# Optimization experiments

Measured on AMD Instinct MI355X. Metric: run time of the kernel, lower is better.

Reference implementation:

```python
import jax, jax.numpy as jnp
import numpy as np

N = 100000      # nodes
E = 1600000     # edges (before self-loops)
IN = 128        # in_channels
HID = 64        # hidden_channels (= out_channels)
HEADS = 8
CH = HID // HEADS  # per-head channels in GAT (concat=True)


def setup_inputs() -> dict:
    key = jax.random.key(0)
    ks = jax.random.split(key, 12)
    s = 0.1  # param init scale
    return {
        "x": jax.random.normal(ks[0], (N, IN), jnp.float32),
        "edge_index": jax.random.randint(ks[1], (2, E), 0, N, dtype=jnp.int32),
        # GCNConv 0: in -> hid
        "W0": s * jax.random.normal(ks[2], (IN, HID), jnp.float32),
        "b0": jnp.zeros((HID,), jnp.float32),
        # GATConv: hid -> heads x ch (concat)
        "Wg": s * jax.random.normal(ks[3], (HID, HEADS * CH), jnp.float32),
        "att_src": s * jax.random.normal(ks[4], (HEADS, CH), jnp.float32),
        "att_dst": s * jax.random.normal(ks[5], (HEADS, CH), jnp.float32),
        "bg": jnp.zeros((HEADS * CH,), jnp.float32),
        # GCNConv 2: hid -> hid
        "W2": s * jax.random.normal(ks[6], (HID, HID), jnp.float32),
        "b2": jnp.zeros((HID,), jnp.float32),
        # GCNConv 3 (final): hid -> out
        "W3": s * jax.random.normal(ks[7], (HID, HID), jnp.float32),
        "b3": jnp.zeros((HID,), jnp.float32),
    }


def _gcn_conv(x, src, dst, W, b, n):
    deg = jax.ops.segment_sum(jnp.ones(src.shape[0], x.dtype), dst, num_segments=n)
    dinv = jnp.where(deg > 0, jax.lax.rsqrt(deg), 0.0)
    h = x @ W                                  # [n, out]
    norm = dinv[src] * dinv[dst]               # [e]
    msg = h[src] * norm[:, None]               # gather + scale
    return jax.ops.segment_sum(msg, dst, num_segments=n) + b


def _gat_conv(x, src, dst, W, a_src, a_dst, b, n):
    # PyG GATConv (v1), concat=True, negative_slope=0.2, self-loops in src/dst
    h = (x @ W).reshape(n, HEADS, CH)          # [n, H, C]
    alpha_src = jnp.sum(h * a_src, axis=-1)    # [n, H]
    alpha_dst = jnp.sum(h * a_dst, axis=-1)    # [n, H]
    e = jax.nn.leaky_relu(alpha_src[src] + alpha_dst[dst], 0.2)  # [E, H]
    # softmax over incoming edges of each destination node
    m = jax.ops.segment_max(e, dst, num_segments=n)              # [n, H]
    p = jnp.exp(e - m[dst])
    z = jax.ops.segment_sum(p, dst, num_segments=n)              # [n, H]
    alpha = p / z[dst]                                           # [E, H]
    out = jax.ops.segment_sum(alpha[:, :, None] * h[src], dst, num_segments=n)  # [n, H, C]
    return out.reshape(n, HEADS * CH) + b


def reference(x, edge_index, W0, b0, Wg, att_src, att_dst, bg, W2, b2, W3, b3):
    n = x.shape[0]
    loops = jnp.arange(n, dtype=edge_index.dtype)
    src = jnp.concatenate([edge_index[0], loops])
    dst = jnp.concatenate([edge_index[1], loops])
    # GCN -> relu -> GAT -> relu -> GCN -> relu -> GCN  (dropout p=0.0 is identity)
    h = jax.nn.relu(_gcn_conv(x, src, dst, W0, b0, n))
    h = jax.nn.relu(_gat_conv(h, src, dst, Wg, att_src, att_dst, bg, n))
    h = jax.nn.relu(_gcn_conv(h, src, dst, W2, b2, n))
    h = _gcn_conv(h, src, dst, W3, b3, n)
    return h
```

## Files before the change

### kernel.cpp

```cpp
#include <hip/hip_runtime.h>
#include <hip/hip_bf16.h>


__device__ __forceinline__ float leaky02(float x) { return x > 0.0f ? x : 0.2f * x; }
__device__ __forceinline__ unsigned short f2bf(float f) {
  unsigned u = __float_as_uint(f);
  u += 0x7FFFu + ((u >> 16) & 1u);
  return (unsigned short)(u >> 16);
}
__device__ __forceinline__ unsigned pkbf(float a, float b) {
  return (unsigned)f2bf(a) | ((unsigned)f2bf(b) << 16);
}
__device__ __forceinline__ float bflo(unsigned d) { return __uint_as_float(d << 16); }
__device__ __forceinline__ float bfhi(unsigned d) { return __uint_as_float(d & 0xFFFF0000u); }

#define NB_PART 256
#define CAP 5120

__global__ __launch_bounds__(1024) void part_kernel(
    const int* __restrict__ src, const int* __restrict__ dst,
    int* __restrict__ gcur, unsigned* __restrict__ part,
    int ne, int nbkt, int chunk) {
  __shared__ int h[512];
  __shared__ int curb[512];
  const int tid = threadIdx.x;
  for (int i = tid; i < nbkt; i += 1024) h[i] = 0;
  __syncthreads();
  const int beg = blockIdx.x * chunk;
  const int end = min(beg + chunk, ne);
  int4 sv0 = {0,0,0,0}, dv0 = {0,0,0,0}, sv1 = {0,0,0,0}, dv1 = {0,0,0,0};
  int nv0 = 0, nv1 = 0;
  {
    int e = beg + 4 * tid;
    if (e < end) {
      nv0 = min(end - e, 4);
      if (nv0 == 4) {
        sv0 = *reinterpret_cast<const int4*>(&src[e]);
        dv0 = *reinterpret_cast<const int4*>(&dst[e]);
      } else {
        if (nv0 > 0) { sv0.x = src[e];     dv0.x = dst[e]; }
        if (nv0 > 1) { sv0.y = src[e + 1]; dv0.y = dst[e + 1]; }
        if (nv0 > 2) { sv0.z = src[e + 2]; dv0.z = dst[e + 2]; }
      }
    }
    e = beg + 4096 + 4 * tid;
    if (e < end) {
      nv1 = min(end - e, 4);
      if (nv1 == 4) {
        sv1 = *reinterpret_cast<const int4*>(&src[e]);
        dv1 = *reinterpret_cast<const int4*>(&dst[e]);
      } else {
        if (nv1 > 0) { sv1.x = src[e];     dv1.x = dst[e]; }
        if (nv1 > 1) { sv1.y = src[e + 1]; dv1.y = dst[e + 1]; }
        if (nv1 > 2) { sv1.z = src[e + 2]; dv1.z = dst[e + 2]; }
      }
    }
  }
  if (nv0 > 0) atomicAdd(&h[dv0.x >> 8], 1);
  if (nv0 > 1) atomicAdd(&h[dv0.y >> 8], 1);
  if (nv0 > 2) atomicAdd(&h[dv0.z >> 8], 1);
  if (nv0 > 3) atomicAdd(&h[dv0.w >> 8], 1);
  if (nv1 > 0) atomicAdd(&h[dv1.x >> 8], 1);
  if (nv1 > 1) atomicAdd(&h[dv1.y >> 8], 1);
  if (nv1 > 2) atomicAdd(&h[dv1.z >> 8], 1);
  if (nv1 > 3) atomicAdd(&h[dv1.w >> 8], 1);
  __syncthreads();
  for (int i = tid; i < nbkt; i += 1024)
    curb[i] = i * CAP + atomicAdd(&gcur[i], h[i]);
  __syncthreads();
  if (nv0 > 0) { int p = atomicAdd(&curb[dv0.x >> 8], 1); part[p] = (unsigned)sv0.x | ((unsigned)(dv0.x & 255) << 24); }
  if (nv0 > 1) { int p = atomicAdd(&curb[dv0.y >> 8], 1); part[p] = (unsigned)sv0.y | ((unsigned)(dv0.y & 255) << 24); }
  if (nv0 > 2) { int p = atomicAdd(&curb[dv0.z >> 8], 1); part[p] = (unsigned)sv0.z | ((unsigned)(dv0.z & 255) << 24); }
  if (nv0 > 3) { int p = atomicAdd(&curb[dv0.w >> 8], 1); part[p] = (unsigned)sv0.w | ((unsigned)(dv0.w & 255) << 24); }
  if (nv1 > 0) { int p = atomicAdd(&curb[dv1.x >> 8], 1); part[p] = (unsigned)sv1.x | ((unsigned)(dv1.x & 255) << 24); }
  if (nv1 > 1) { int p = atomicAdd(&curb[dv1.y >> 8], 1); part[p] = (unsigned)sv1.y | ((unsigned)(dv1.y & 255) << 24); }
  if (nv1 > 2) { int p = atomicAdd(&curb[dv1.z >> 8], 1); part[p] = (unsigned)sv1.z | ((unsigned)(dv1.z & 255) << 24); }
  if (nv1 > 3) { int p = atomicAdd(&curb[dv1.w >> 8], 1); part[p] = (unsigned)sv1.w | ((unsigned)(dv1.w & 255) << 24); }
}

__global__ __launch_bounds__(256) void build_kernel(
    const unsigned* __restrict__ part, const int* __restrict__ gcur,
    int2* __restrict__ begcnt, int* __restrict__ csr, float* __restrict__ dinv,
    int n) {
  __shared__ int cnt[256], sc[256], cur[256];
  const int b = blockIdx.x, tid = threadIdx.x;
  const int lo = b << 8;
  const int base = b * CAP;
  const int bcnt = min(gcur[b], CAP);
  cnt[tid] = 0;
  __syncthreads();
  for (int e = tid; e < bcnt; e += 256) atomicAdd(&cnt[part[base + e] >> 24], 1);
  __syncthreads();
  sc[tid] = cnt[tid];
  __syncthreads();
  for (int off = 1; off < 256; off <<= 1) {
    int u = (tid >= off) ? sc[tid - off] : 0;
    __syncthreads();
    sc[tid] += u;
    __syncthreads();
  }
  const int excl = sc[tid] - cnt[tid];
  const int node = lo + tid;
  if (node < n) {
    begcnt[node] = make_int2(base + excl, cnt[tid]);
    dinv[node] = rsqrtf((float)(cnt[tid] + 1));
  }
  cur[tid] = base + excl;
  __syncthreads();
  for (int e = tid; e < bcnt; e += 256) {
    unsigned p = part[base + e];
    int pos = atomicAdd(&cur[p >> 24], 1);
    csr[pos] = (int)(p & 0x00FFFFFFu);
  }
}

template<int K, bool SCALE, bool ABF16, bool FUSEA>
__global__ __launch_bounds__(256) void matmul_kernel(
    const void* __restrict__ Ain, const float* __restrict__ W,
    const float* __restrict__ dinv, unsigned short* __restrict__ C,
    const float* __restrict__ attS, const float* __restrict__ attD,
    float* __restrict__ asrc, float* __restrict__ adst, int n) {
  __shared__ float sW[K * 64];
  __shared__ float sA[64 * (K + 1)];
  const int tid = threadIdx.x;
  const int row0 = blockIdx.x * 64;
  for (int i = tid; i < K * 16; i += 256)
    reinterpret_cast<float4*>(sW)[i] = reinterpret_cast<const float4*>(W)[i];
  if constexpr (!ABF16) {
    const float* A = (const float*)Ain;
    const int f4r = K / 4;
    for (int i = tid; i < 64 * f4r; i += 256) {
      int r = i / f4r, f = i - r * f4r;
      int row = row0 + r;
      float4 v = (row < n)
          ? reinterpret_cast<const float4*>(&A[(long)row * K])[f]
          : make_float4(0.f, 0.f, 0.f, 0.f);
      float* p = &sA[r * (K + 1) + f * 4];
      p[0] = v.x; p[1] = v.y; p[2] = v.z; p[3] = v.w;
    }
  } else {
    const unsigned short* A = (const unsigned short*)Ain;
    const int f8r = K / 8;
    for (int i = tid; i < 64 * f8r; i += 256) {
      int r = i / f8r, f = i - r * f8r;
      int row = row0 + r;
      uint4 v = (row < n)
          ? *reinterpret_cast<const uint4*>(&A[(long)row * K + f * 8])
          : make_uint4(0, 0, 0, 0);
      float* p = &sA[r * (K + 1) + f * 8];
      p[0] = bflo(v.x); p[1] = bfhi(v.x); p[2] = bflo(v.y); p[3] = bfhi(v.y);
      p[4] = bflo(v.z); p[5] = bfhi(v.z); p[6] = bflo(v.w); p[7] = bfhi(v.w);
    }
  }
  __syncthreads();
  const int tc = tid & 15, tr = tid >> 4;
  const int c0 = tc * 4, r0 = tr * 4;
  float4 acc0 = {0,0,0,0}, acc1 = {0,0,0,0}, acc2 = {0,0,0,0}, acc3 = {0,0,0,0};
  const float* a0 = &sA[(r0 + 0) * (K + 1)];
  const float* a1 = &sA[(r0 + 1) * (K + 1)];
  const float* a2 = &sA[(r0 + 2) * (K + 1)];
  const float* a3 = &sA[(r0 + 3) * (K + 1)];
#pragma unroll 8
  for (int k = 0; k < K; ++k) {
    float4 w = *reinterpret_cast<const float4*>(&sW[k * 64 + c0]);
    float x0 = a0[k], x1 = a1[k], x2 = a2[k], x3 = a3[k];
    acc0.x = fmaf(x0, w.x, acc0.x); acc0.y = fmaf(x0, w.y, acc0.y);
    acc0.z = fmaf(x0, w.z, acc0.z); acc0.w = fmaf(x0, w.w, acc0.w);
    acc1.x = fmaf(x1, w.x, acc1.x); acc1.y = fmaf(x1, w.y, acc1.y);
    acc1.z = fmaf(x1, w.z, acc1.z); acc1.w = fmaf(x1, w.w, acc1.w);
    acc2.x = fmaf(x2, w.x, acc2.x); acc2.y = fmaf(x2, w.y, acc2.y);
    acc2.z = fmaf(x2, w.z, acc2.z); acc2.w = fmaf(x2, w.w, acc2.w);
    acc3.x = fmaf(x3, w.x, acc3.x); acc3.y = fmaf(x3, w.y, acc3.y);
    acc3.z = fmaf(x3, w.z, acc3.z); acc3.w = fmaf(x3, w.w, acc3.w);
  }
  float4 accs[4] = {acc0, acc1, acc2, acc3};
#pragma unroll
  for (int i = 0; i < 4; ++i) {
    int row = row0 + r0 + i;
    float s = SCALE ? ((row < n) ? dinv[row] : 1.0f) : 1.0f;
    float v0 = accs[i].x * s, v1 = accs[i].y * s;
    float v2 = accs[i].z * s, v3 = accs[i].w * s;
    if constexpr (FUSEA) {
      float ps = fmaf(v0, attS[c0], fmaf(v1, attS[c0 + 1],
                 fmaf(v2, attS[c0 + 2], v3 * attS[c0 + 3])));
      float pd = fmaf(v0, attD[c0], fmaf(v1, attD[c0 + 1],
                 fmaf(v2, attD[c0 + 2], v3 * attD[c0 + 3])));
      ps += __shfl_xor(ps, 1);
      pd += __shfl_xor(pd, 1);
      if (row < n && (tc & 1) == 0) {
        int h = tc >> 1;
        asrc[(long)row * 8 + h] = ps;
        adst[(long)row * 8 + h] = pd;
      }
    }
    if (row < n) {
      uint2 o;
      o.x = pkbf(v0, v1);
      o.y = pkbf(v2, v3);
      *reinterpret_cast<uint2*>(&C[(long)row * 64 + c0]) = o;
    }
  }
}

template<bool RELU, bool OBF16>
__global__ __launch_bounds__(256) void gcn_layer_kernel(
    const int2* __restrict__ begcnt, const int* __restrict__ csr,
    const unsigned short* __restrict__ hs, const float* __restrict__ dinv,
    const float* __restrict__ bias, void* __restrict__ out, int n) {
  int node = blockIdx.x * 4 + (threadIdx.x >> 6);
  if (node >= n) return;
  int lane = threadIdx.x & 63;
  int slot = lane >> 3;
  int li = lane & 7;
  int c0 = li * 8;
  int2 bc = begcnt[node];
  int beg = bc.x, end = bc.x + bc.y;
  float4 accA = {0,0,0,0}, accB = {0,0,0,0};
  int j = beg;
  int idx = (j + li < end) ? csr[j + li] : 0;
  while (j < end) {
    int s = __shfl(idx, slot);
    bool valid = (j + slot) < end;
    int jn = j + 8;
    if (jn < end) idx = (jn + li < end) ? csr[jn + li] : 0;
    if (valid) {
      uint4 v = *reinterpret_cast<const uint4*>(&hs[(long)s * 64 + c0]);
      accA.x += bflo(v.x); accA.y += bfhi(v.x);
      accA.z += bflo(v.y); accA.w += bfhi(v.y);
      accB.x += bflo(v.z); accB.y += bfhi(v.z);
      accB.z += bflo(v.w); accB.w += bfhi(v.w);
    }
    j = jn;
  }
  if (slot == 0) {
    uint4 v = *reinterpret_cast<const uint4*>(&hs[(long)node * 64 + c0]);
    accA.x += bflo(v.x); accA.y += bfhi(v.x);
    accA.z += bflo(v.y); accA.w += bfhi(v.y);
    accB.x += bflo(v.z); accB.y += bfhi(v.z);
    accB.z += bflo(v.w); accB.w += bfhi(v.w);
  }
#pragma unroll
  for (int m = 8; m <= 32; m <<= 1) {
    accA.x += __shfl_xor(accA.x, m); accA.y += __shfl_xor(accA.y, m);
    accA.z += __shfl_xor(accA.z, m); accA.w += __shfl_xor(accA.w, m);
    accB.x += __shfl_xor(accB.x, m); accB.y += __shfl_xor(accB.y, m);
    accB.z += __shfl_xor(accB.z, m); accB.w += __shfl_xor(accB.w, m);
  }
  if (slot == 0) {
    float sdv = dinv[node];
    float4 bbA = *reinterpret_cast<const float4*>(&bias[c0]);
    float4 bbB = *reinterpret_cast<const float4*>(&bias[c0 + 4]);
    float o0 = fmaf(sdv, accA.x, bbA.x), o1 = fmaf(sdv, accA.y, bbA.y);
    float o2 = fmaf(sdv, accA.z, bbA.z), o3 = fmaf(sdv, accA.w, bbA.w);
    float o4 = fmaf(sdv, accB.x, bbB.x), o5 = fmaf(sdv, accB.y, bbB.y);
    float o6 = fmaf(sdv, accB.z, bbB.z), o7 = fmaf(sdv, accB.w, bbB.w);
    if (RELU) {
      o0 = fmaxf(o0, 0.f); o1 = fmaxf(o1, 0.f); o2 = fmaxf(o2, 0.f);
      o3 = fmaxf(o3, 0.f); o4 = fmaxf(o4, 0.f); o5 = fmaxf(o5, 0.f);
      o6 = fmaxf(o6, 0.f); o7 = fmaxf(o7, 0.f);
    }
    if constexpr (OBF16) {
      unsigned short* op = (unsigned short*)out;
      uint4 q;
      q.x = pkbf(o0, o1); q.y = pkbf(o2, o3);
      q.z = pkbf(o4, o5); q.w = pkbf(o6, o7);
      *reinterpret_cast<uint4*>(&op[(long)node * 64 + c0]) = q;
    } else {
      float* op = (float*)out;
      *reinterpret_cast<float4*>(&op[(long)node * 64 + c0]) =
          make_float4(o0, o1, o2, o3);
      *reinterpret_cast<float4*>(&op[(long)node * 64 + c0 + 4]) =
          make_float4(o4, o5, o6, o7);
    }
  }
}

__global__ __launch_bounds__(256) void gat_layer_kernel(
    const int2* __restrict__ begcnt, const int* __restrict__ csr,
    const unsigned short* __restrict__ hg, const float* __restrict__ asrc,
    const float* __restrict__ adst, const float* __restrict__ bg,
    unsigned short* __restrict__ out, int n) {
  int node = blockIdx.x * 4 + (threadIdx.x >> 6);
  if (node >= n) return;
  int lane = threadIdx.x & 63;
  int slot = lane >> 3;
  int li = lane & 7;
  int c0 = li * 8;
  int h = li;
  int2 bc = begcnt[node];
  int beg = bc.x, end = bc.x + bc.y;
  float adn = adst[node * 8 + h];
  float4 accA = {0,0,0,0}, accB = {0,0,0,0};
  float z = 0.f;
  int j = beg;
  int idx = (j + li < end) ? csr[j + li] : 0;
  while (j < end) {
    int s = __shfl(idx, slot);
    bool valid = (j + slot) < end;
    int jn = j + 8;
    if (jn < end) idx = (jn + li < end) ? csr[jn + li] : 0;
    if (valid) {
      float p = __expf(leaky02(asrc[s * 8 + h] + adn));
      uint4 v = *reinterpret_cast<const uint4*>(&hg[(long)s * 64 + c0]);
      z += p;
      accA.x = fmaf(p, bflo(v.x), accA.x); accA.y = fmaf(p, bfhi(v.x), accA.y);
      accA.z = fmaf(p, bflo(v.y), accA.z); accA.w = fmaf(p, bfhi(v.y), accA.w);
      accB.x = fmaf(p, bflo(v.z), accB.x); accB.y = fmaf(p, bfhi(v.z), accB.y);
      accB.z = fmaf(p, bflo(v.w), accB.z); accB.w = fmaf(p, bfhi(v.w), accB.w);
    }
    j = jn;
  }
  if (slot == 0) {
    float p = __expf(leaky02(asrc[node * 8 + h] + adn));
    uint4 v = *reinterpret_cast<const uint4*>(&hg[(long)node * 64 + c0]);
    z += p;
    accA.x = fmaf(p, bflo(v.x), accA.x); accA.y = fmaf(p, bfhi(v.x), accA.y);
    accA.z = fmaf(p, bflo(v.y), accA.z); accA.w = fmaf(p, bfhi(v.y), accA.w);
    accB.x = fmaf(p, bflo(v.z), accB.x); accB.y = fmaf(p, bfhi(v.z), accB.y);
    accB.z = fmaf(p, bflo(v.w), accB.z); accB.w = fmaf(p, bfhi(v.w), accB.w);
  }
#pragma unroll
  for (int m = 8; m <= 32; m <<= 1) {
    accA.x += __shfl_xor(accA.x, m); accA.y += __shfl_xor(accA.y, m);
    accA.z += __shfl_xor(accA.z, m); accA.w += __shfl_xor(accA.w, m);
    accB.x += __shfl_xor(accB.x, m); accB.y += __shfl_xor(accB.y, m);
    accB.z += __shfl_xor(accB.z, m); accB.w += __shfl_xor(accB.w, m);
    z += __shfl_xor(z, m);
  }
  if (slot == 0) {
    float rz = 1.0f / z;
    float4 bbA = *reinterpret_cast<const float4*>(&bg[c0]);
    float4 bbB = *reinterpret_cast<const float4*>(&bg[c0 + 4]);
    float o0 = fmaxf(fmaf(accA.x, rz, bbA.x), 0.f);
    float o1 = fmaxf(fmaf(accA.y, rz, bbA.y), 0.f);
    float o2 = fmaxf(fmaf(accA.z, rz, bbA.z), 0.f);
    float o3 = fmaxf(fmaf(accA.w, rz, bbA.w), 0.f);
    float o4 = fmaxf(fmaf(accB.x, rz, bbB.x), 0.f);
    float o5 = fmaxf(fmaf(accB.y, rz, bbB.y), 0.f);
    float o6 = fmaxf(fmaf(accB.z, rz, bbB.z), 0.f);
    float o7 = fmaxf(fmaf(accB.w, rz, bbB.w), 0.f);
    uint4 q;
    q.x = pkbf(o0, o1); q.y = pkbf(o2, o3);
    q.z = pkbf(o4, o5); q.w = pkbf(o6, o7);
    *reinterpret_cast<uint4*>(&out[(long)node * 64 + c0]) = q;
  }
}

extern "C" void kernel_launch(void* const* d_in, const int* in_sizes, int n_in,
                              void* d_out, int out_size, void* d_ws, size_t ws_size,
                              hipStream_t stream) {
  const float* x  = (const float*)d_in[0];
  const int* ei   = (const int*)d_in[1];
  const float* W0 = (const float*)d_in[2];
  const float* b0 = (const float*)d_in[3];
  const float* Wg = (const float*)d_in[4];
  const float* av = (const float*)d_in[5];
  const float* aw = (const float*)d_in[6];
  const float* bg = (const float*)d_in[7];
  const float* W2 = (const float*)d_in[8];
  const float* b2 = (const float*)d_in[9];
  const float* W3 = (const float*)d_in[10];
  const float* b3 = (const float*)d_in[11];

  const int N = in_sizes[0] / 128;
  const int E = in_sizes[1] / 2;
  const int* src = ei;
  const int* dst = ei + E;
  const int nbkt = (N + 255) >> 8;
  const int chunk = (((E + NB_PART - 1) / NB_PART) + 3) & ~3;

  char* base = (char*)d_ws;
  size_t off = 0;
  auto alloc = [&](size_t bytes) {
    void* p = base + off;
    off = (off + bytes + 255) & ~(size_t)255;
    return p;
  };
  int*   gcur    = (int*)alloc((size_t)nbkt * 4);
  int2*  begcnt  = (int2*)alloc((size_t)N * 8);
  int*   csr     = (int*)alloc((size_t)nbkt * CAP * 4);
  float* dinv    = (float*)alloc((size_t)N * 4);
  float* as_     = (float*)alloc((size_t)N * 8 * 4);
  float* ad_     = (float*)alloc((size_t)N * 8 * 4);
  unsigned short* fStd = (unsigned short*)alloc((size_t)N * 64 * 2);
  unsigned short* aggB = (unsigned short*)alloc((size_t)N * 64 * 2);
  unsigned* part = (unsigned*)alloc((size_t)nbkt * CAP * 4);
  (void)ws_size; (void)n_in; (void)out_size;

  const int gMM   = (N + 63) / 64;
  const int gNode = (N + 3) / 4;

  hipMemsetAsync(gcur, 0, (size_t)nbkt * 4, stream);
  part_kernel<<<NB_PART, 1024, 0, stream>>>(src, dst, gcur, part, E, nbkt, chunk);
  build_kernel<<<nbkt, 256, 0, stream>>>(part, gcur, begcnt, csr, dinv, N);

  matmul_kernel<128, true, false, false><<<gMM, 256, 0, stream>>>(
      x, W0, dinv, fStd, nullptr, nullptr, nullptr, nullptr, N);
  gcn_layer_kernel<true, true><<<gNode, 256, 0, stream>>>(
      begcnt, csr, fStd, dinv, b0, aggB, N);

  matmul_kernel<64, false, true, true><<<gMM, 256, 0, stream>>>(
      aggB, Wg, nullptr, fStd, av, aw, as_, ad_, N);
  gat_layer_kernel<<<gNode, 256, 0, stream>>>(
      begcnt, csr, fStd, as_, ad_, bg, aggB, N);

  matmul_kernel<64, true, true, false><<<gMM, 256, 0, stream>>>(
      aggB, W2, dinv, fStd, nullptr, nullptr, nullptr, nullptr, N);
  gcn_layer_kernel<true, true><<<gNode, 256, 0, stream>>>(
      begcnt, csr, fStd, dinv, b2, aggB, N);

  matmul_kernel<64, true, true, false><<<gMM, 256, 0, stream>>>(
      aggB, W3, dinv, fStd, nullptr, nullptr, nullptr, nullptr, N);
  gcn_layer_kernel<false, false><<<gNode, 256, 0, stream>>>(
      begcnt, csr, fStd, dinv, b3, d_out, N);
}
```

Before: 439.5 us.

## Use bf16 MFMA for 64-wide matmuls and pad CSR rows to multiples of eight

Replaces the scalar FMA matmul for the three K=64 layers with a kernel built on the mfma_f32_16x16x32_bf16 instruction, which stages bf16 weights in shared memory and also fuses the GAT attention dot products. The CSR build now pads each node's neighbor list to a multiple of eight, using a dummy node index n whose features are zero and whose attention source is -1e30. The aggregation loops can then drop their per-edge bounds checks and predication. In exchange the weights are rounded to bf16, the CSR buffer grows, and extra padded gathers of the dummy row are added.

```diff
diff --git a/kernel.cpp b/kernel.cpp
--- a/kernel.cpp
+++ b/kernel.cpp
@@ -14,8 +14,12 @@
 __device__ __forceinline__ float bflo(unsigned d) { return __uint_as_float(d << 16); }
 __device__ __forceinline__ float bfhi(unsigned d) { return __uint_as_float(d & 0xFFFF0000u); }
 
+typedef __attribute__((ext_vector_type(8))) short short8;
+typedef __attribute__((ext_vector_type(4))) float f32x4;
+
 #define NB_PART 256
-#define CAP 5120
+#define CAP_P 5120
+#define CAP_C 7168
 
 __global__ __launch_bounds__(1024) void part_kernel(
     const int* __restrict__ src, const int* __restrict__ dst,
@@ -66,7 +70,7 @@
   if (nv1 > 3) atomicAdd(&h[dv1.w >> 8], 1);
   __syncthreads();
   for (int i = tid; i < nbkt; i += 1024)
-    curb[i] = i * CAP + atomicAdd(&gcur[i], h[i]);
+    curb[i] = i * CAP_P + atomicAdd(&gcur[i], h[i]);
   __syncthreads();
   if (nv0 > 0) { int p = atomicAdd(&curb[dv0.x >> 8], 1); part[p] = (unsigned)sv0.x | ((unsigned)(dv0.x & 255) << 24); }
   if (nv0 > 1) { int p = atomicAdd(&curb[dv0.y >> 8], 1); part[p] = (unsigned)sv0.y | ((unsigned)(dv0.y & 255) << 24); }
@@ -81,17 +85,21 @@
 __global__ __launch_bounds__(256) void build_kernel(
     const unsigned* __restrict__ part, const int* __restrict__ gcur,
     int2* __restrict__ begcnt, int* __restrict__ csr, float* __restrict__ dinv,
-    int n) {
+    unsigned short* __restrict__ fStd, float* __restrict__ as_,
+    float* __restrict__ ad_, int n) {
   __shared__ int cnt[256], sc[256], cur[256];
   const int b = blockIdx.x, tid = threadIdx.x;
   const int lo = b << 8;
-  const int base = b * CAP;
-  const int bcnt = min(gcur[b], CAP);
+  const int basep = b * CAP_P;
+  const int basec = b * CAP_C;
+  const int bcnt = min(gcur[b], CAP_P);
   cnt[tid] = 0;
   __syncthreads();
-  for (int e = tid; e < bcnt; e += 256) atomicAdd(&cnt[part[base + e] >> 24], 1);
-  __syncthreads();
-  sc[tid] = cnt[tid];
+  for (int e = tid; e < bcnt; e += 256) atomicAdd(&cnt[part[basep + e] >> 24], 1);
+  __syncthreads();
+  const int cn = cnt[tid];
+  const int cp = (cn + 7) & ~7;
+  sc[tid] = cp;
   __syncthreads();
   for (int off = 1; off < 256; off <<= 1) {
     int u = (tid >= off) ? sc[tid - off] : 0;
@@ -99,58 +107,47 @@
     sc[tid] += u;
     __syncthreads();
   }
-  const int excl = sc[tid] - cnt[tid];
+  const int excl = sc[tid] - cp;
   const int node = lo + tid;
+  const int beg = basec + excl;
   if (node < n) {
-    begcnt[node] = make_int2(base + excl, cnt[tid]);
-    dinv[node] = rsqrtf((float)(cnt[tid] + 1));
-  }
-  cur[tid] = base + excl;
+    begcnt[node] = make_int2(beg, cn);
+    dinv[node] = rsqrtf((float)(cn + 1));
+  }
+  cur[tid] = beg;
   __syncthreads();
   for (int e = tid; e < bcnt; e += 256) {
-    unsigned p = part[base + e];
+    unsigned p = part[basep + e];
     int pos = atomicAdd(&cur[p >> 24], 1);
     csr[pos] = (int)(p & 0x00FFFFFFu);
   }
-}
-
-template<int K, bool SCALE, bool ABF16, bool FUSEA>
+  __syncthreads();
+  for (int k = cn; k < cp; ++k) csr[beg + k] = n;
+  if (b == 0) {
+    if (tid < 64) fStd[(long)n * 64 + tid] = 0;
+    if (tid < 8) { as_[(long)n * 8 + tid] = -1e30f; ad_[(long)n * 8 + tid] = 0.f; }
+  }
+}
+
+template<int K, bool SCALE>
 __global__ __launch_bounds__(256) void matmul_kernel(
-    const void* __restrict__ Ain, const float* __restrict__ W,
-    const float* __restrict__ dinv, unsigned short* __restrict__ C,
-    const float* __restrict__ attS, const float* __restrict__ attD,
-    float* __restrict__ asrc, float* __restrict__ adst, int n) {
+    const float* __restrict__ A, const float* __restrict__ W,
+    const float* __restrict__ dinv, unsigned short* __restrict__ C, int n) {
   __shared__ float sW[K * 64];
   __shared__ float sA[64 * (K + 1)];
   const int tid = threadIdx.x;
   const int row0 = blockIdx.x * 64;
   for (int i = tid; i < K * 16; i += 256)
     reinterpret_cast<float4*>(sW)[i] = reinterpret_cast<const float4*>(W)[i];
-  if constexpr (!ABF16) {
-    const float* A = (const float*)Ain;
-    const int f4r = K / 4;
-    for (int i = tid; i < 64 * f4r; i += 256) {
-      int r = i / f4r, f = i - r * f4r;
-      int row = row0 + r;
-      float4 v = (row < n)
-          ? reinterpret_cast<const float4*>(&A[(long)row * K])[f]
-          : make_float4(0.f, 0.f, 0.f, 0.f);
-      float* p = &sA[r * (K + 1) + f * 4];
-      p[0] = v.x; p[1] = v.y; p[2] = v.z; p[3] = v.w;
-    }
-  } else {
-    const unsigned short* A = (const unsigned short*)Ain;
-    const int f8r = K / 8;
-    for (int i = tid; i < 64 * f8r; i += 256) {
-      int r = i / f8r, f = i - r * f8r;
-      int row = row0 + r;
-      uint4 v = (row < n)
-          ? *reinterpret_cast<const uint4*>(&A[(long)row * K + f * 8])
-          : make_uint4(0, 0, 0, 0);
-      float* p = &sA[r * (K + 1) + f * 8];
-      p[0] = bflo(v.x); p[1] = bfhi(v.x); p[2] = bflo(v.y); p[3] = bfhi(v.y);
-      p[4] = bflo(v.z); p[5] = bfhi(v.z); p[6] = bflo(v.w); p[7] = bfhi(v.w);
-    }
+  const int f4r = K / 4;
+  for (int i = tid; i < 64 * f4r; i += 256) {
+    int r = i / f4r, f = i - r * f4r;
+    int row = row0 + r;
+    float4 v = (row < n)
+        ? reinterpret_cast<const float4*>(&A[(long)row * K])[f]
+        : make_float4(0.f, 0.f, 0.f, 0.f);
+    float* p = &sA[r * (K + 1) + f * 4];
+    p[0] = v.x; p[1] = v.y; p[2] = v.z; p[3] = v.w;
   }
   __syncthreads();
   const int tc = tid & 15, tr = tid >> 4;
@@ -177,28 +174,93 @@
 #pragma unroll
   for (int i = 0; i < 4; ++i) {
     int row = row0 + r0 + i;
-    float s = SCALE ? ((row < n) ? dinv[row] : 1.0f) : 1.0f;
-    float v0 = accs[i].x * s, v1 = accs[i].y * s;
-    float v2 = accs[i].z * s, v3 = accs[i].w * s;
+    if (row < n) {
+      float s = SCALE ? dinv[row] : 1.0f;
+      uint2 o;
+      o.x = pkbf(accs[i].x * s, accs[i].y * s);
+      o.y = pkbf(accs[i].z * s, accs[i].w * s);
+      *reinterpret_cast<uint2*>(&C[(long)row * 64 + c0]) = o;
+    }
+  }
+}
+
+template<bool SCALE, bool FUSEA>
+__global__ __launch_bounds__(256) void mfma_mm_kernel(
+    const unsigned short* __restrict__ A, const float* __restrict__ W,
+    const float* __restrict__ dinv, unsigned short* __restrict__ C,
+    const float* __restrict__ attS, const float* __restrict__ attD,
+    float* __restrict__ asrc, float* __restrict__ adst, int n) {
+  __shared__ short sB[512 * 8];
+  __shared__ float sC[4][16][68];
+  const int tid = threadIdx.x;
+  const int row0 = blockIdx.x * 64;
+  for (int s = tid; s < 512; s += 256) {
+    int nt = s >> 7, ks = (s >> 6) & 1, l = s & 63;
+    int col = nt * 16 + (l & 15);
+    int kb = ks * 32 + ((l >> 4) << 3);
+    short8 wv;
+#pragma unroll
+    for (int j = 0; j < 8; ++j)
+      wv[j] = (short)f2bf(W[(kb + j) * 64 + col]);
+    *reinterpret_cast<short8*>(&sB[s * 8]) = wv;
+  }
+  __syncthreads();
+  const int w = tid >> 6;
+  const int l = tid & 63;
+  const int rw = row0 + w * 16;
+  int arow = rw + (l & 15);
+  int arowc = min(arow, n - 1);
+  const unsigned short* ap = &A[(long)arowc * 64 + ((l >> 4) << 3)];
+  short8 a0 = *reinterpret_cast<const short8*>(ap);
+  short8 a1 = *reinterpret_cast<const short8*>(ap + 32);
+  f32x4 acc[4];
+#pragma unroll
+  for (int nt = 0; nt < 4; ++nt) {
+    f32x4 c = {0.f, 0.f, 0.f, 0.f};
+    short8 b0 = *reinterpret_cast<const short8*>(&sB[((nt * 2 + 0) * 64 + l) * 8]);
+    short8 b1 = *reinterpret_cast<const short8*>(&sB[((nt * 2 + 1) * 64 + l) * 8]);
+    c = __builtin_amdgcn_mfma_f32_16x16x32_bf16(a0, b0, c, 0, 0, 0);
+    c = __builtin_amdgcn_mfma_f32_16x16x32_bf16(a1, b1, c, 0, 0, 0);
+    acc[nt] = c;
+  }
+#pragma unroll
+  for (int nt = 0; nt < 4; ++nt)
+#pragma unroll
+    for (int r = 0; r < 4; ++r)
+      sC[w][(l >> 4) * 4 + r][nt * 16 + (l & 15)] = acc[nt][r];
+  __syncthreads();
+  int row16 = l & 15, ch = l >> 4;
+  int orow = rw + row16;
+  if (orow < n) {
+    float v[16];
+#pragma unroll
+    for (int q = 0; q < 4; ++q) {
+      float4 t = *reinterpret_cast<const float4*>(&sC[w][row16][ch * 16 + q * 4]);
+      v[q * 4 + 0] = t.x; v[q * 4 + 1] = t.y;
+      v[q * 4 + 2] = t.z; v[q * 4 + 3] = t.w;
+    }
     if constexpr (FUSEA) {
-      float ps = fmaf(v0, attS[c0], fmaf(v1, attS[c0 + 1],
-                 fmaf(v2, attS[c0 + 2], v3 * attS[c0 + 3])));
-      float pd = fmaf(v0, attD[c0], fmaf(v1, attD[c0 + 1],
-                 fmaf(v2, attD[c0 + 2], v3 * attD[c0 + 3])));
-      ps += __shfl_xor(ps, 1);
-      pd += __shfl_xor(pd, 1);
-      if (row < n && (tc & 1) == 0) {
-        int h = tc >> 1;
-        asrc[(long)row * 8 + h] = ps;
-        adst[(long)row * 8 + h] = pd;
+      float ps0 = 0, pd0 = 0, ps1 = 0, pd1 = 0;
+#pragma unroll
+      for (int q = 0; q < 8; ++q) {
+        ps0 = fmaf(v[q], attS[ch * 16 + q], ps0);
+        pd0 = fmaf(v[q], attD[ch * 16 + q], pd0);
+        ps1 = fmaf(v[8 + q], attS[ch * 16 + 8 + q], ps1);
+        pd1 = fmaf(v[8 + q], attD[ch * 16 + 8 + q], pd1);
       }
-    }
-    if (row < n) {
-      uint2 o;
-      o.x = pkbf(v0, v1);
-      o.y = pkbf(v2, v3);
-      *reinterpret_cast<uint2*>(&C[(long)row * 64 + c0]) = o;
-    }
+      asrc[(long)orow * 8 + ch * 2] = ps0;
+      adst[(long)orow * 8 + ch * 2] = pd0;
+      asrc[(long)orow * 8 + ch * 2 + 1] = ps1;
+      adst[(long)orow * 8 + ch * 2 + 1] = pd1;
+    }
+    float s = SCALE ? dinv[orow] : 1.0f;
+    uint4 q0, q1;
+    q0.x = pkbf(v[0] * s, v[1] * s);   q0.y = pkbf(v[2] * s, v[3] * s);
+    q0.z = pkbf(v[4] * s, v[5] * s);   q0.w = pkbf(v[6] * s, v[7] * s);
+    q1.x = pkbf(v[8] * s, v[9] * s);   q1.y = pkbf(v[10] * s, v[11] * s);
+    q1.z = pkbf(v[12] * s, v[13] * s); q1.w = pkbf(v[14] * s, v[15] * s);
+    *reinterpret_cast<uint4*>(&C[(long)orow * 64 + ch * 16]) = q0;
+    *reinterpret_cast<uint4*>(&C[(long)orow * 64 + ch * 16 + 8]) = q1;
   }
 }
 
@@ -214,22 +276,19 @@
   int li = lane & 7;
   int c0 = li * 8;
   int2 bc = begcnt[node];
-  int beg = bc.x, end = bc.x + bc.y;
+  int beg = bc.x, end = bc.x + ((bc.y + 7) & ~7);
   float4 accA = {0,0,0,0}, accB = {0,0,0,0};
   int j = beg;
-  int idx = (j + li < end) ? csr[j + li] : 0;
+  int idx = csr[j + li];
   while (j < end) {
     int s = __shfl(idx, slot);
-    bool valid = (j + slot) < end;
     int jn = j + 8;
-    if (jn < end) idx = (jn + li < end) ? csr[jn + li] : 0;
-    if (valid) {
-      uint4 v = *reinterpret_cast<const uint4*>(&hs[(long)s * 64 + c0]);
-      accA.x += bflo(v.x); accA.y += bfhi(v.x);
-      accA.z += bflo(v.y); accA.w += bfhi(v.y);
-      accB.x += bflo(v.z); accB.y += bfhi(v.z);
-      accB.z += bflo(v.w); accB.w += bfhi(v.w);
-    }
+    idx = csr[jn + li];
+    uint4 v = *reinterpret_cast<const uint4*>(&hs[(long)s * 64 + c0]);
+    accA.x += bflo(v.x); accA.y += bfhi(v.x);
+    accA.z += bflo(v.y); accA.w += bfhi(v.y);
+    accB.x += bflo(v.z); accB.y += bfhi(v.z);
+    accB.z += bflo(v.w); accB.w += bfhi(v.w);
     j = jn;
   }
   if (slot == 0) {
@@ -288,26 +347,23 @@
   int c0 = li * 8;
   int h = li;
   int2 bc = begcnt[node];
-  int beg = bc.x, end = bc.x + bc.y;
+  int beg = bc.x, end = bc.x + ((bc.y + 7) & ~7);
   float adn = adst[node * 8 + h];
   float4 accA = {0,0,0,0}, accB = {0,0,0,0};
   float z = 0.f;
   int j = beg;
-  int idx = (j + li < end) ? csr[j + li] : 0;
+  int idx = csr[j + li];
   while (j < end) {
     int s = __shfl(idx, slot);
-    bool valid = (j + slot) < end;
     int jn = j + 8;
-    if (jn < end) idx = (jn + li < end) ? csr[jn + li] : 0;
-    if (valid) {
-      float p = __expf(leaky02(asrc[s * 8 + h] + adn));
-      uint4 v = *reinterpret_cast<const uint4*>(&hg[(long)s * 64 + c0]);
-      z += p;
-      accA.x = fmaf(p, bflo(v.x), accA.x); accA.y = fmaf(p, bfhi(v.x), accA.y);
-      accA.z = fmaf(p, bflo(v.y), accA.z); accA.w = fmaf(p, bfhi(v.y), accA.w);
-      accB.x = fmaf(p, bflo(v.z), accB.x); accB.y = fmaf(p, bfhi(v.z), accB.y);
-      accB.z = fmaf(p, bflo(v.w), accB.z); accB.w = fmaf(p, bfhi(v.w), accB.w);
-    }
+    idx = csr[jn + li];
+    float p = __expf(leaky02(asrc[s * 8 + h] + adn));
+    uint4 v = *reinterpret_cast<const uint4*>(&hg[(long)s * 64 + c0]);
+    z += p;
+    accA.x = fmaf(p, bflo(v.x), accA.x); accA.y = fmaf(p, bfhi(v.x), accA.y);
+    accA.z = fmaf(p, bflo(v.y), accA.z); accA.w = fmaf(p, bfhi(v.y), accA.w);
+    accB.x = fmaf(p, bflo(v.z), accB.x); accB.y = fmaf(p, bfhi(v.z), accB.y);
+    accB.z = fmaf(p, bflo(v.w), accB.z); accB.w = fmaf(p, bfhi(v.w), accB.w);
     j = jn;
   }
   if (slot == 0) {
@@ -378,13 +434,13 @@
   };
   int*   gcur    = (int*)alloc((size_t)nbkt * 4);
   int2*  begcnt  = (int2*)alloc((size_t)N * 8);
-  int*   csr     = (int*)alloc((size_t)nbkt * CAP * 4);
+  int*   csr     = (int*)alloc(((size_t)nbkt * CAP_C + 64) * 4);
   float* dinv    = (float*)alloc((size_t)N * 4);
-  float* as_     = (float*)alloc((size_t)N * 8 * 4);
-  float* ad_     = (float*)alloc((size_t)N * 8 * 4);
-  unsigned short* fStd = (unsigned short*)alloc((size_t)N * 64 * 2);
+  float* as_     = (float*)alloc((size_t)(N + 1) * 8 * 4);
+  float* ad_     = (float*)alloc((size_t)(N + 1) * 8 * 4);
+  unsigned short* fStd = (unsigned short*)alloc(((size_t)N * 64 + 64) * 2);
   unsigned short* aggB = (unsigned short*)alloc((size_t)N * 64 * 2);
-  unsigned* part = (unsigned*)alloc((size_t)nbkt * CAP * 4);
+  unsigned* part = (unsigned*)alloc((size_t)nbkt * CAP_P * 4);
   (void)ws_size; (void)n_in; (void)out_size;
 
   const int gMM   = (N + 63) / 64;
@@ -392,24 +448,24 @@
 
   hipMemsetAsync(gcur, 0, (size_t)nbkt * 4, stream);
   part_kernel<<<NB_PART, 1024, 0, stream>>>(src, dst, gcur, part, E, nbkt, chunk);
-  build_kernel<<<nbkt, 256, 0, stream>>>(part, gcur, begcnt, csr, dinv, N);
-
-  matmul_kernel<128, true, false, false><<<gMM, 256, 0, stream>>>(
-      x, W0, dinv, fStd, nullptr, nullptr, nullptr, nullptr, N);
+  build_kernel<<<nbkt, 256, 0, stream>>>(part, gcur, begcnt, csr, dinv,
+                                         fStd, as_, ad_, N);
+
+  matmul_kernel<128, true><<<gMM, 256, 0, stream>>>(x, W0, dinv, fStd, N);
   gcn_layer_kernel<true, true><<<gNode, 256, 0, stream>>>(
       begcnt, csr, fStd, dinv, b0, aggB, N);
 
-  matmul_kernel<64, false, true, true><<<gMM, 256, 0, stream>>>(
+  mfma_mm_kernel<false, true><<<gMM, 256, 0, stream>>>(
       aggB, Wg, nullptr, fStd, av, aw, as_, ad_, N);
   gat_layer_kernel<<<gNode, 256, 0, stream>>>(
       begcnt, csr, fStd, as_, ad_, bg, aggB, N);
 
-  matmul_kernel<64, true, true, false><<<gMM, 256, 0, stream>>>(
+  mfma_mm_kernel<true, false><<<gMM, 256, 0, stream>>>(
       aggB, W2, dinv, fStd, nullptr, nullptr, nullptr, nullptr, N);
   gcn_layer_kernel<true, true><<<gNode, 256, 0, stream>>>(
       begcnt, csr, fStd, dinv, b2, aggB, N);
 
-  matmul_kernel<64, true, true, false><<<gMM, 256, 0, stream>>>(
+  mfma_mm_kernel<true, false><<<gMM, 256, 0, stream>>>(
       aggB, W3, dinv, fStd, nullptr, nullptr, nullptr, nullptr, N);
   gcn_layer_kernel<false, false><<<gNode, 256, 0, stream>>>(
       begcnt, csr, fStd, dinv, b3, d_out, N);
```

New measurement: 430.8 us. 1.02x faster.
